# Optimization experiments

Hardware: AMD Instinct MI355X
Metric: run time of the kernel (lower is better)

## Reference

```python
import jax, jax.numpy as jnp
import numpy as np
from jax import lax

# OpenCV GaussianBlur(ksize=5, sigma=0) uses the fixed tabulated kernel [1,4,6,4,1]/16
_G1 = np.array([1.0, 4.0, 6.0, 4.0, 1.0], np.float32) / 16.0
GAUSS_K = jnp.asarray(np.outer(_G1, _G1))  # (5,5)
_D2 = np.array([1.0, 0.0, -2.0, 0.0, 1.0], np.float32)
_S = np.array([1.0, 4.0, 6.0, 4.0, 1.0], np.float32)
LAP_K = jnp.asarray(np.outer(_S, _D2) + np.outer(_D2, _S))  # (5,5)


def _conv2d_reflect101(img, k):
    # img: (N, h, w); k: (5,5). OpenCV default border = BORDER_REFLECT_101 == jnp 'reflect'
    p = jnp.pad(img, ((0, 0), (2, 2), (2, 2)), mode='reflect')
    out = lax.conv_general_dilated(p[:, None], k[None, None], (1, 1), 'VALID')
    return out[:, 0]


def reference(x):
    b, s, c, h, w = x.shape
    # grayscale per image: mean over channels
    g = x.mean(axis=2).reshape(b * s, h, w)
    blurred = _conv2d_reflect101(g, GAUSS_K)
    lap = _conv2d_reflect101(blurred, LAP_K).reshape(b, s, h, w)
    # sharpest frame per pixel (laplacian replicated over channels in original,
    # so argmax is channel-independent)
    idx = jnp.argmax(lap, axis=1)  # (b, h, w)
    idx = jnp.broadcast_to(idx[:, None, None, :, :], (b, 1, c, h, w))
    merged = jnp.take_along_axis(x, idx, axis=1)[:, 0]  # (b, c, h, w)
    return merged


def setup_inputs() -> dict:
    key = jax.random.key(0)
    x = jax.random.normal(key, (4, 8, 3, 1024, 1024), dtype=jnp.float32)
    return {"x": x}
```

## Files before the change

### kernel.cpp

```cpp
#include <hip/hip_runtime.h>

#define BB 4
#define SS 8
#define CC 3
#define HH 1024
#define WW 1024
#define TH 32
#define TW 64
#define GSH (TH + 8)
#define GSW (TW + 8)
#define BLH (TH + 4)
#define BLW (TW + 4)
#define NSTRIP 3
#define RBS 12
#define HBS (RBS + 4)
#define NSLOT (NSTRIP * BLW)

__device__ __forceinline__ int refl(int i, int n) {
    i = (i < 0) ? -i : i;
    i = (i >= n) ? (2 * n - 2 - i) : i;
    return i;
}

__global__ __launch_bounds__(256, 6)
void lap_focus_fused(const float* __restrict__ x, float* __restrict__ out) {
    const int tile = blockIdx.x;
    const int b  = tile >> 9;
    const int t  = tile & 511;
    const int tr = t >> 4;
    const int tc = t & 15;
    const int r0 = tr * TH;
    const int c0 = tc * TW;

    __shared__ float gs[GSH][GSW];
    __shared__ float bl[BLH][BLW];

    const int tid = threadIdx.x;
    const int tx = tid & 63;
    const int ty = tid >> 6;

    float best[8];
    int   bidx[8];
#pragma unroll
    for (int m = 0; m < 8; ++m) { best[m] = -3.0e38f; bidx[m] = 0; }

    const double GA[5] = {0.0625, 0.25, 0.375, 0.25, 0.0625};
    const double LW[5][5] = {
        { 2.,  4.,   4.,  4.,  2.},
        { 4.,  0.,  -8.,  0.,  4.},
        { 4., -8., -24., -8.,  4.},
        { 4.,  0.,  -8.,  0.,  4.},
        { 2.,  4.,   4.,  4.,  2.},
    };

    int ccol[5];
#pragma unroll
    for (int dj = 0; dj < 5; ++dj)
        ccol[dj] = refl(c0 + tx + dj - 2, WW) - c0 + 2;

    const bool slot_active = (tid < NSLOT);
    const int strip = tid / BLW;
    const int scol  = tid - strip * BLW;
    const int hr0   = strip * RBS;

    const size_t HW = (size_t)HH * WW;

    auto load_gray = [&](int s) {
        const float* xs = x + (size_t)((b * SS + s) * CC) * HW;
        for (int e = tid; e < GSH * GSW; e += 256) {
            int r = e / GSW;
            int c = e - r * GSW;
            int gi = refl(r0 + r - 4, HH);
            int gj = refl(c0 + c - 4, WW);
            size_t off = (size_t)gi * WW + gj;
            float v = (xs[off] + xs[HW + off]) + xs[2 * HW + off];
            gs[r][c] = v / 3.0f;
        }
    };

    load_gray(0);
    __syncthreads();

    for (int s = 0; s < SS; ++s) {
        if (slot_active) {
            double w[5];
#pragma unroll
            for (int k = 0; k < HBS; ++k) {
                double acc = 0.0;
#pragma unroll
                for (int j = 0; j < 5; ++j)
                    acc += (double)gs[hr0 + k][scol + j] * GA[j];
                w[k % 5] = acc;
                if (k >= 4) {
                    const int rb = k - 4;
                    double a2 = 0.0;
#pragma unroll
                    for (int i = 0; i < 5; ++i)
                        a2 += w[(rb + i) % 5] * GA[i];
                    bl[hr0 + rb][scol] = (float)a2;
                }
            }
        }
        __syncthreads();

        if (s + 1 < SS) load_gray(s + 1);

#pragma unroll
        for (int m = 0; m < 8; ++m) {
            int i = ty + 4 * m;
            double acc = 0.0;
#pragma unroll
            for (int di = 0; di < 5; ++di) {
                int rr = refl(r0 + i + di - 2, HH) - r0 + 2;
#pragma unroll
                for (int dj = 0; dj < 5; ++dj) {
                    if (LW[di][dj] != 0.0)
                        acc += (double)bl[rr][ccol[dj]] * LW[di][dj];
                }
            }
            float lap = (float)acc;
            if (lap > best[m]) { best[m] = lap; bidx[m] = s; }
        }
        __syncthreads();
    }

#pragma unroll
    for (int m = 0; m < 8; ++m) {
        int i = ty + 4 * m;
        int gi = r0 + i;
        int gj = c0 + tx;
        size_t off = (size_t)gi * WW + gj;
        const float* xs = x + (size_t)((b * SS + bidx[m]) * CC) * HW + off;
        float* op = out + (size_t)(b * CC) * HW + off;
        op[0]      = xs[0];
        op[HW]     = xs[HW];
        op[2 * HW] = xs[2 * HW];
    }
}

extern "C" void kernel_launch(void* const* d_in, const int* in_sizes, int n_in,
                              void* d_out, int out_size, void* d_ws, size_t ws_size,
                              hipStream_t stream) {
    (void)in_sizes; (void)n_in; (void)d_ws; (void)ws_size; (void)out_size;
    const float* x = (const float*)d_in[0];
    float* out = (float*)d_out;
    dim3 grid(BB * (HH / TH) * (WW / TW));
    dim3 block(256);
    hipLaunchKernelGGL(lap_focus_fused, grid, block, 0, stream, x, out);
}
```

Measured before the change: 788.4 us.

## Vectorize interior gray loads and slide register window for Laplacian rows

Interior tiles now load the three channels with float4 reads and skip reflection index math. The Laplacian stage gives each thread 8 consecutive rows and keeps a rolling 5-row register window, so each new row needs only 5 shared reads instead of 25. The loop barriers are rearranged so the next frame's gray load follows the Laplacian directly, without a separate sync between them. Launch bounds drop to 4 blocks per SM, allowing more registers for the window at the cost of occupancy.

```diff
diff --git a/kernel.cpp b/kernel.cpp
--- a/kernel.cpp
+++ b/kernel.cpp
@@ -22,8 +22,8 @@
     return i;
 }
 
-__global__ __launch_bounds__(256, 6)
-void lap_focus_fused(const float* __restrict__ x, float* __restrict__ out) {
+__global__ __launch_bounds__(256, 4)
+void lap_focus_v3(const float* __restrict__ x, float* __restrict__ out) {
     const int tile = blockIdx.x;
     const int b  = tile >> 9;
     const int t  = tile & 511;
@@ -32,7 +32,7 @@
     const int r0 = tr * TH;
     const int c0 = tc * TW;
 
-    __shared__ float gs[GSH][GSW];
+    __shared__ __align__(16) float gs[GSH][GSW];
     __shared__ float bl[BLH][BLW];
 
     const int tid = threadIdx.x;
@@ -63,25 +63,47 @@
     const int scol  = tid - strip * BLW;
     const int hr0   = strip * RBS;
 
+    const bool rowInterior = (tr != 0) && (tr != 31);
+    const bool colInterior = (tc != 0) && (tc != 15);
+
     const size_t HW = (size_t)HH * WW;
 
     auto load_gray = [&](int s) {
         const float* xs = x + (size_t)((b * SS + s) * CC) * HW;
-        for (int e = tid; e < GSH * GSW; e += 256) {
-            int r = e / GSW;
-            int c = e - r * GSW;
-            int gi = refl(r0 + r - 4, HH);
-            int gj = refl(c0 + c - 4, WW);
-            size_t off = (size_t)gi * WW + gj;
-            float v = (xs[off] + xs[HW + off]) + xs[2 * HW + off];
-            gs[r][c] = v / 3.0f;
+        if (rowInterior && colInterior) {
+            const float* basep = xs + (size_t)(r0 - 4) * WW + (c0 - 4);
+            for (int e = tid; e < GSH * (GSW / 4); e += 256) {
+                int r  = e / (GSW / 4);
+                int c4 = (e - r * (GSW / 4)) * 4;
+                const float* p = basep + (size_t)r * WW + c4;
+                const float4 a  = *reinterpret_cast<const float4*>(p);
+                const float4 b2 = *reinterpret_cast<const float4*>(p + HW);
+                const float4 c2 = *reinterpret_cast<const float4*>(p + 2 * HW);
+                float4 v;
+                v.x = ((a.x + b2.x) + c2.x) / 3.0f;
+                v.y = ((a.y + b2.y) + c2.y) / 3.0f;
+                v.z = ((a.z + b2.z) + c2.z) / 3.0f;
+                v.w = ((a.w + b2.w) + c2.w) / 3.0f;
+                *reinterpret_cast<float4*>(&gs[r][c4]) = v;
+            }
+        } else {
+            for (int e = tid; e < GSH * GSW; e += 256) {
+                int r = e / GSW;
+                int c = e - r * GSW;
+                int gi = refl(r0 + r - 4, HH);
+                int gj = refl(c0 + c - 4, WW);
+                size_t off = (size_t)gi * WW + gj;
+                float v = (xs[off] + xs[HW + off]) + xs[2 * HW + off];
+                gs[r][c] = v / 3.0f;
+            }
         }
     };
 
     load_gray(0);
-    __syncthreads();
 
     for (int s = 0; s < SS; ++s) {
+        __syncthreads();
+
         if (slot_active) {
             double w[5];
 #pragma unroll
@@ -103,30 +125,59 @@
         }
         __syncthreads();
 
+        if (rowInterior) {
+            float cw[5][5];
+#pragma unroll
+            for (int di = 0; di < 5; ++di)
+#pragma unroll
+                for (int dj = 0; dj < 5; ++dj)
+                    cw[di][dj] = bl[8 * ty + di][ccol[dj]];
+#pragma unroll
+            for (int m = 0; m < 8; ++m) {
+                double acc = 0.0;
+#pragma unroll
+                for (int di = 0; di < 5; ++di) {
+                    const int sl = (m + di) % 5;
+#pragma unroll
+                    for (int dj = 0; dj < 5; ++dj) {
+                        if (LW[di][dj] != 0.0)
+                            acc += (double)cw[sl][dj] * LW[di][dj];
+                    }
+                }
+                float lap = (float)acc;
+                if (lap > best[m]) { best[m] = lap; bidx[m] = s; }
+                if (m < 7) {
+                    const int sl2 = m % 5;
+#pragma unroll
+                    for (int dj = 0; dj < 5; ++dj)
+                        cw[sl2][dj] = bl[8 * ty + m + 5][ccol[dj]];
+                }
+            }
+        } else {
+#pragma unroll
+            for (int m = 0; m < 8; ++m) {
+                int i = 8 * ty + m;
+                double acc = 0.0;
+#pragma unroll
+                for (int di = 0; di < 5; ++di) {
+                    int rr = refl(r0 + i + di - 2, HH) - r0 + 2;
+#pragma unroll
+                    for (int dj = 0; dj < 5; ++dj) {
+                        if (LW[di][dj] != 0.0)
+                            acc += (double)bl[rr][ccol[dj]] * LW[di][dj];
+                    }
+                }
+                float lap = (float)acc;
+                if (lap > best[m]) { best[m] = lap; bidx[m] = s; }
+            }
+        }
+
         if (s + 1 < SS) load_gray(s + 1);
-
-#pragma unroll
-        for (int m = 0; m < 8; ++m) {
-            int i = ty + 4 * m;
-            double acc = 0.0;
-#pragma unroll
-            for (int di = 0; di < 5; ++di) {
-                int rr = refl(r0 + i + di - 2, HH) - r0 + 2;
-#pragma unroll
-                for (int dj = 0; dj < 5; ++dj) {
-                    if (LW[di][dj] != 0.0)
-                        acc += (double)bl[rr][ccol[dj]] * LW[di][dj];
-                }
-            }
-            float lap = (float)acc;
-            if (lap > best[m]) { best[m] = lap; bidx[m] = s; }
-        }
-        __syncthreads();
     }
 
 #pragma unroll
     for (int m = 0; m < 8; ++m) {
-        int i = ty + 4 * m;
+        int i = 8 * ty + m;
         int gi = r0 + i;
         int gj = c0 + tx;
         size_t off = (size_t)gi * WW + gj;
@@ -146,5 +197,5 @@
     float* out = (float*)d_out;
     dim3 grid(BB * (HH / TH) * (WW / TW));
     dim3 block(256);
-    hipLaunchKernelGGL(lap_focus_fused, grid, block, 0, stream, x, out);
+    hipLaunchKernelGGL(lap_focus_v3, grid, block, 0, stream, x, out);
 }
```

New measurement: 817.0 us. 3.6% more time.
